# Performance work log

Hardware: AMD Instinct MI355X
Metric: run time of the kernel (lower is better)

Reference implementation:

```python
import jax, jax.numpy as jnp
import numpy as np

EMB = 1024
DM = 64
NH = 16

def setup_inputs() -> dict:
    key = jax.random.key(0)
    ks = jax.random.split(key, 11)
    bs, slen = 2, 2048
    s = 1.0 / np.sqrt(EMB)
    inp = {
        'Q': jax.random.normal(ks[0], (bs, slen, EMB), jnp.float32),
        'K': jax.random.normal(ks[1], (bs, slen, EMB), jnp.float32),
        'V': jax.random.normal(ks[2], (bs, slen, EMB), jnp.float32),
        'Wq': jax.random.normal(ks[3], (EMB, DM * NH), jnp.float32) * s,
        'bq': jnp.zeros((DM * NH,), jnp.float32),
        'Wk': jax.random.normal(ks[4], (EMB, DM * NH), jnp.float32) * s,
        'bk': jnp.zeros((DM * NH,), jnp.float32),
        'Wv': jax.random.normal(ks[5], (EMB, DM * NH), jnp.float32) * s,
        'bv': jnp.zeros((DM * NH,), jnp.float32),
        'Wo': jax.random.normal(ks[6], (DM * NH, EMB), jnp.float32) * (1.0 / np.sqrt(DM * NH)),
        'bo': jnp.zeros((EMB,), jnp.float32),
    }
    return inp

def reference(Q, K, V, Wq, bq, Wk, bk, Wv, bv, Wo, bo):
    bs, q_len, _ = Q.shape
    kv_len = K.shape[1]
    scale = 1.0 / np.sqrt(DM)
    # project and split heads: (n, l, h, d)
    q = (scale * (Q @ Wq + bq)).reshape(bs, q_len, NH, DM)
    k = (K @ Wk + bk).reshape(bs, kv_len, NH, DM)
    v = (V @ Wv + bv).reshape(bs, kv_len, NH, DM)
    # scores (n, h, l, s) -- full S x S matrix, as in the original
    qk = jnp.einsum('nlhd,nshd->nhls', q, k)
    a = jax.nn.softmax(qk, axis=-1)  # dropout p=0 -> identity
    o = jnp.einsum('nhls,nshd->nlhd', a, v).reshape(bs, q_len, NH * DM)
    return o @ Wo + bo
```

## Files before the change

### kernel.cpp

```cpp
#include <hip/hip_runtime.h>
#include <cstdint>
#include <cstddef>

#define EMB  1024
#define DM   64
#define NH   16
#define SLEN 2048
#define BS   2

typedef _Float16 f16x8 __attribute__((ext_vector_type(8)));
typedef _Float16 f16x4 __attribute__((ext_vector_type(4)));
typedef __fp16   hf2   __attribute__((ext_vector_type(2)));
typedef __fp16   hf4   __attribute__((ext_vector_type(4)));
typedef __fp16   hf8   __attribute__((ext_vector_type(8)));
typedef float    f32x4 __attribute__((ext_vector_type(4)));

#define ASYNC_LD16(gp, lp)                                                        \
    __builtin_amdgcn_global_load_lds(                                             \
        (const __attribute__((address_space(1))) void*)(gp),                      \
        (__attribute__((address_space(3))) void*)(lp), 16, 0, 0)

__global__ __launch_bounds__(256)
void prep(const float* __restrict__ Wq, const float* __restrict__ Wk,
          const float* __restrict__ Wv, const float* __restrict__ Wo,
          _Float16* __restrict__ WqT, _Float16* __restrict__ WkT,
          _Float16* __restrict__ WvT, _Float16* __restrict__ WoT)
{
    __shared__ float t[64][65];
    const float* W;
    _Float16*    T;
    switch (blockIdx.z) {
        case 0:  W = Wq; T = WqT; break;
        case 1:  W = Wk; T = WkT; break;
        case 2:  W = Wv; T = WvT; break;
        default: W = Wo; T = WoT; break;
    }
    const int tid = threadIdx.x;
    const int bn  = (blockIdx.x & 15) * 64;
    const int bk  = (blockIdx.x >> 4) * 64;

    #pragma unroll
    for (int p = 0; p < 4; ++p) {
        int row = p * 16 + (tid >> 4);
        int col = (tid & 15) * 4;
        float4 v = *(const float4*)(W + (size_t)(bk + row) * EMB + bn + col);
        t[row][col+0] = v.x; t[row][col+1] = v.y; t[row][col+2] = v.z; t[row][col+3] = v.w;
    }
    __syncthreads();
    #pragma unroll
    for (int p = 0; p < 4; ++p) {
        int nr = p * 16 + (tid >> 4);
        int kc = (tid & 15) * 4;
        f16x4 o;
        o[0] = (_Float16)t[kc+0][nr];
        o[1] = (_Float16)t[kc+1][nr];
        o[2] = (_Float16)t[kc+2][nr];
        o[3] = (_Float16)t[kc+3][nr];
        *(f16x4*)&T[(size_t)(bn + nr) * EMB + bk + kc] = o;
    }
}

template <bool A32>
__device__ __forceinline__
void gemm_core(const void* __restrict__ Aptr, const _Float16* __restrict__ Bt,
               const float* __restrict__ bias, float* __restrict__ Cf,
               _Float16* __restrict__ Ch, int M, int N, int K,
               float scale, int mode, int bx, int by)
{
    __shared__ __align__(16) _Float16 As[2][64 * 64];
    __shared__ __align__(16) _Float16 Bs[2][128 * 64];

    const int tid  = threadIdx.x;
    const int lane = tid & 63;
    const int wave = tid >> 6;
    const int c    = lane & 15;
    const int quad = lane >> 4;
    const int bm   = by * 64;
    const int bn   = bx * 128;
    const int wm   = (wave >> 1) * 32;
    const int wn   = (wave & 1) * 64;

    f32x4 acc[2][4];
    #pragma unroll
    for (int i = 0; i < 2; ++i)
        #pragma unroll
        for (int j = 0; j < 4; ++j)
            #pragma unroll
            for (int r = 0; r < 4; ++r) acc[i][j][r] = 0.f;

    const size_t Kb = (size_t)K * 2;
    const int    lc = ((tid & 7) ^ ((tid >> 3) & 7)) * 16;
    const char* gB = (const char*)Bt + (size_t)(bn + (tid >> 3)) * Kb + lc;

    const char*  gA16 = nullptr;
    const float* gA32 = nullptr;
    int aswz0 = 0, aswz1 = 0;
    if constexpr (A32) {
        const int ar  = tid >> 2;
        const int acg = tid & 3;
        gA32  = (const float*)Aptr + (size_t)(bm + ar) * K + acg * 16;
        aswz0 = ar * 64 + (((2*acg    ) ^ (ar & 7)) * 8);
        aswz1 = ar * 64 + (((2*acg + 1) ^ (ar & 7)) * 8);
    } else {
        gA16 = (const char*)Aptr + (size_t)(bm + (tid >> 3)) * Kb + lc;
    }

    const int NS = K / 64;

    auto stageB = [&](int buf, int t) {
        const size_t ko = (size_t)t * 128;
        char* lB = (char*)&Bs[buf][0] + wave * 1024;
        ASYNC_LD16(gB + ko,           lB);
        ASYNC_LD16(gB + 32*Kb + ko,   lB + 4096);
        ASYNC_LD16(gB + 64*Kb + ko,   lB + 8192);
        ASYNC_LD16(gB + 96*Kb + ko,   lB + 12288);
    };
    auto stageA16 = [&](int buf, int t) {
        const size_t ko = (size_t)t * 128;
        char* lA = (char*)&As[buf][0] + wave * 1024;
        ASYNC_LD16(gA16 + ko,         lA);
        ASYNC_LD16(gA16 + 32*Kb + ko, lA + 4096);
    };
    auto writeA32 = [&](int buf, const float4& a0, const float4& a1,
                        const float4& a2, const float4& a3) {
        f16x8 h0, h1;
        h0[0] = (_Float16)a0.x; h0[1] = (_Float16)a0.y;
        h0[2] = (_Float16)a0.z; h0[3] = (_Float16)a0.w;
        h0[4] = (_Float16)a1.x; h0[5] = (_Float16)a1.y;
        h0[6] = (_Float16)a1.z; h0[7] = (_Float16)a1.w;
        h1[0] = (_Float16)a2.x; h1[1] = (_Float16)a2.y;
        h1[2] = (_Float16)a2.z; h1[3] = (_Float16)a2.w;
        h1[4] = (_Float16)a3.x; h1[5] = (_Float16)a3.y;
        h1[6] = (_Float16)a3.z; h1[7] = (_Float16)a3.w;
        *(f16x8*)&As[buf][aswz0] = h0;
        *(f16x8*)&As[buf][aswz1] = h1;
    };

    if constexpr (A32) {
        float4 a0 = *(const float4*)(gA32 + 0);
        float4 a1 = *(const float4*)(gA32 + 4);
        float4 a2 = *(const float4*)(gA32 + 8);
        float4 a3 = *(const float4*)(gA32 + 12);
        stageB(0, 0);
        writeA32(0, a0, a1, a2, a3);
    } else {
        stageA16(0, 0);
        stageB(0, 0);
    }
    __syncthreads();

    int cur = 0;
    for (int t = 0; t < NS; ++t) {
        float4 a0, a1, a2, a3;
        if constexpr (A32) {
            if (t + 1 < NS) {
                const float* p = gA32 + (size_t)(t + 1) * 64;
                a0 = *(const float4*)(p + 0);
                a1 = *(const float4*)(p + 4);
                a2 = *(const float4*)(p + 8);
                a3 = *(const float4*)(p + 12);
            }
        }
        if (t + 1 < NS) {
            if constexpr (!A32) stageA16(cur ^ 1, t + 1);
            stageB(cur ^ 1, t + 1);
        }

        #pragma unroll
        for (int kk = 0; kk < 2; ++kk) {
            f16x8 af[2], bf[4];
            #pragma unroll
            for (int i = 0; i < 2; ++i)
                af[i] = *(const f16x8*)
                    &As[cur][(wm + i*16 + c) * 64 + (((kk*4 + quad) ^ (c & 7)) * 8)];
            #pragma unroll
            for (int j = 0; j < 4; ++j)
                bf[j] = *(const f16x8*)
                    &Bs[cur][(wn + j*16 + c) * 64 + (((kk*4 + quad) ^ (c & 7)) * 8)];
            #pragma unroll
            for (int i = 0; i < 2; ++i)
                #pragma unroll
                for (int j = 0; j < 4; ++j)
                    acc[i][j] = __builtin_amdgcn_mfma_f32_16x16x32_f16(af[i], bf[j], acc[i][j], 0, 0, 0);
        }

        if constexpr (A32) {
            if (t + 1 < NS) writeA32(cur ^ 1, a0, a1, a2, a3);
        }
        __syncthreads();
        cur ^= 1;
    }

    float bcol[4];
    #pragma unroll
    for (int j = 0; j < 4; ++j) bcol[j] = bias[bn + wn + j * 16 + c];

    #pragma unroll
    for (int i = 0; i < 2; ++i) {
        int m0 = bm + wm + i * 16 + quad * 4;
        #pragma unroll
        for (int j = 0; j < 4; ++j) {
            int n = bn + wn + j * 16 + c;
            if (mode == 0) {
                #pragma unroll
                for (int r = 0; r < 4; ++r)
                    Cf[(size_t)(m0 + r) * N + n] = acc[i][j][r] + bcol[j];
            } else if (mode == 1) {
                int h = n >> 6, d = n & 63;
                #pragma unroll
                for (int r = 0; r < 4; ++r) {
                    int mm = m0 + r;
                    int b = mm >> 11, l = mm & (SLEN - 1);
                    Ch[(((size_t)(b * NH + h)) * SLEN + l) * DM + d] =
                        (_Float16)((acc[i][j][r] + bcol[j]) * scale);
                }
            } else {
                int h = n >> 6, d = n & 63;
                int b = m0 >> 11, l = m0 & (SLEN - 1);
                f16x4 o;
                #pragma unroll
                for (int r = 0; r < 4; ++r)
                    o[r] = (_Float16)(acc[i][j][r] + bcol[j]);
                *(f16x4*)&Ch[(((size_t)(b * NH + h)) * DM + d) * SLEN + l] = o;
            }
        }
    }
}

__device__ __forceinline__ void xcd_swz(int& bx, int& by)
{
    int wid = blockIdx.x + 8 * blockIdx.y;
    bx = wid >> 6;
    by = wid & 63;
}

__global__ __launch_bounds__(256)
void gemm_qkv(const float* __restrict__ Q, const float* __restrict__ K,
              const float* __restrict__ V,
              const _Float16* __restrict__ WqT, const _Float16* __restrict__ WkT,
              const _Float16* __restrict__ WvT,
              const float* __restrict__ bq, const float* __restrict__ bk,
              const float* __restrict__ bv,
              _Float16* __restrict__ q_ws, _Float16* __restrict__ k_ws,
              _Float16* __restrict__ v_ws)
{
    const float* A;
    const _Float16* Bt;
    const float* bias;
    _Float16* Ch;
    float scale;
    int mode;
    if (blockIdx.z == 0)      { A = Q; Bt = WqT; bias = bq; Ch = q_ws; scale = 0.18033688f; mode = 1; }
    else if (blockIdx.z == 1) { A = K; Bt = WkT; bias = bk; Ch = k_ws; scale = 1.0f;        mode = 1; }
    else                      { A = V; Bt = WvT; bias = bv; Ch = v_ws; scale = 1.0f;        mode = 2; }
    int bx, by; xcd_swz(bx, by);
    gemm_core<true>(A, Bt, bias, nullptr, Ch, BS * SLEN, NH * DM, EMB, scale, mode, bx, by);
}

__global__ __launch_bounds__(256)
void gemm_out(const _Float16* __restrict__ Oh, const _Float16* __restrict__ WoT,
              const float* __restrict__ bo, float* __restrict__ out)
{
    int bx, by; xcd_swz(bx, by);
    gemm_core<false>(Oh, WoT, bo, out, nullptr, BS * SLEN, EMB, NH * DM, 1.0f, 0, bx, by);
}

__global__ __launch_bounds__(512)
void attn_mfma(const _Float16* __restrict__ qw, const _Float16* __restrict__ kw,
               const _Float16* __restrict__ vwT, _Float16* __restrict__ ow)
{
    __shared__ __align__(16) _Float16 Kt[4][64 * 64];
    __shared__ __align__(16) _Float16 Vt[4][64 * 64];

    const int tid  = threadIdx.x;
    const int lane = tid & 63;
    const int wave = tid >> 6;
    const int c    = lane & 15;
    const int quad = lane >> 4;
    const int qg   = wave & 3;
    const int kh   = wave >> 2;
    const int bh   = blockIdx.y;
    const int b    = bh >> 4;
    const int h    = bh & 15;
    const int qbase = blockIdx.x * 128 + qg * 32;

    const _Float16* kb = kw  + (size_t)bh * SLEN * DM;
    const _Float16* vb = vwT + (size_t)bh * DM * SLEN;
    const _Float16* qb = qw  + (size_t)bh * SLEN * DM;

    f16x8 qf[2][2];
    #pragma unroll
    for (int t = 0; t < 2; ++t)
        #pragma unroll
        for (int ch = 0; ch < 2; ++ch)
            qf[t][ch] = *(const f16x8*)(qb + (size_t)(qbase + t*16 + c) * DM + ch*32 + quad*8);

    f32x4 oacc[2][4];
    f32x4 lacc[2];
    #pragma unroll
    for (int t = 0; t < 2; ++t) {
        #pragma unroll
        for (int dg = 0; dg < 4; ++dg)
            #pragma unroll
            for (int r = 0; r < 4; ++r) oacc[t][dg][r] = 0.f;
        #pragma unroll
        for (int r = 0; r < 4; ++r) lacc[t][r] = 0.f;
    }

    const f16x8 ones8 = {(_Float16)1.f, (_Float16)1.f, (_Float16)1.f, (_Float16)1.f,
                         (_Float16)1.f, (_Float16)1.f, (_Float16)1.f, (_Float16)1.f};
    const f32x4 zero4 = {0.f, 0.f, 0.f, 0.f};

    const int r0  = wave * 8 + (lane >> 3);
    const int lc0 = (((lane & 7) ^ ((lane >> 3) & 7)) * 16);
    const char* gk = (const char*)kb + r0 * 128 + lc0;
    const char* gv = (const char*)vb + (size_t)r0 * 4096 + lc0;

    auto stage = [&](int buf) {
        char* pk = (char*)&Kt[buf][0] + wave * 1024;
        char* pv = (char*)&Vt[buf][0] + wave * 1024;
        ASYNC_LD16(gk, pk);
        ASYNC_LD16(gv, pv);
        gk += 8192;
        gv += 128;
    };

    stage(0); stage(1); stage(2);
    asm volatile("s_waitcnt vmcnt(4)" ::: "memory");
    __builtin_amdgcn_s_barrier();
    asm volatile("" ::: "memory");

    const int NT = SLEN / 64;
    for (int t = 0; t < NT; ++t) {
        stage((t + 3) & 3);
        const int cb = t & 3;

        f16x8 kf[2][2];
        #pragma unroll
        for (int kg = 0; kg < 2; ++kg)
            #pragma unroll
            for (int ch = 0; ch < 2; ++ch)
                kf[kg][ch] = *(const f16x8*)
                    &Kt[cb][(kh*32 + kg*16 + c) * 64 + (((ch*4 + quad) ^ (c & 7)) * 8)];

        f32x4 s[2][2];
        #pragma unroll
        for (int t2 = 0; t2 < 2; ++t2)
            #pragma unroll
            for (int kg = 0; kg < 2; ++kg) {
                s[t2][kg] = __builtin_amdgcn_mfma_f32_16x16x32_f16(kf[kg][0], qf[t2][0], zero4,     0, 0, 0);
                s[t2][kg] = __builtin_amdgcn_mfma_f32_16x16x32_f16(kf[kg][1], qf[t2][1], s[t2][kg], 0, 0, 0);
            }

        f16x8 pf8[2];
        #pragma unroll
        for (int t2 = 0; t2 < 2; ++t2) {
            hf4 h4[2];
            #pragma unroll
            for (int u = 0; u < 2; ++u) {
                float p0 = __builtin_amdgcn_exp2f(s[t2][u][0]);
                float p1 = __builtin_amdgcn_exp2f(s[t2][u][1]);
                float p2 = __builtin_amdgcn_exp2f(s[t2][u][2]);
                float p3 = __builtin_amdgcn_exp2f(s[t2][u][3]);
                hf2 lo = __builtin_amdgcn_cvt_pkrtz(p0, p1);
                hf2 hi = __builtin_amdgcn_cvt_pkrtz(p2, p3);
                h4[u] = __builtin_shufflevector(lo, hi, 0, 1, 2, 3);
            }
            hf8 h8 = __builtin_shufflevector(h4[0], h4[1], 0, 1, 2, 3, 4, 5, 6, 7);
            pf8[t2] = __builtin_bit_cast(f16x8, h8);
        }

        #pragma unroll
        for (int t2 = 0; t2 < 2; ++t2)
            lacc[t2] = __builtin_amdgcn_mfma_f32_16x16x32_f16(pf8[t2], ones8, lacc[t2], 0, 0, 0);

        #pragma unroll
        for (int dg = 0; dg < 4; ++dg) {
            f16x4 vf[2];
            #pragma unroll
            for (int u = 0; u < 2; ++u)
                vf[u] = *(const f16x4*)
                    &Vt[cb][(dg*16 + c) * 64 +
                            (((kh*4 + 2*u + (quad >> 1)) ^ (c & 7)) * 8) + (quad & 1) * 4];
            f16x8 v8 = __builtin_shufflevector(vf[0], vf[1], 0, 1, 2, 3, 4, 5, 6, 7);
            #pragma unroll
            for (int t2 = 0; t2 < 2; ++t2)
                oacc[t2][dg] = __builtin_amdgcn_mfma_f32_16x16x32_f16(pf8[t2], v8, oacc[t2][dg], 0, 0, 0);
        }

        asm volatile("s_waitcnt vmcnt(4)" ::: "memory");
        __builtin_amdgcn_s_barrier();
        asm volatile("" ::: "memory");
    }

    __syncthreads();

    float* mb = (float*)&Kt[0][0];
    #pragma unroll
    for (int t = 0; t < 2; ++t) {
        if (kh == 1) {
            float* p = mb + ((qg * 64 + lane) * 20);
            *(f32x4*)(p +  0) = oacc[t][0];
            *(f32x4*)(p +  4) = oacc[t][1];
            *(f32x4*)(p +  8) = oacc[t][2];
            *(f32x4*)(p + 12) = oacc[t][3];
            *(f32x4*)(p + 16) = lacc[t];
        }
        __syncthreads();
        if (kh == 0) {
            const float* p = mb + ((qg * 64 + lane) * 20);
            f32x4 po[4], pl;
            po[0] = *(const f32x4*)(p +  0);
            po[1] = *(const f32x4*)(p +  4);
            po[2] = *(const f32x4*)(p +  8);
            po[3] = *(const f32x4*)(p + 12);
            pl    = *(const f32x4*)(p + 16);
            #pragma unroll
            for (int r = 0; r < 4; ++r) {
                float linv = 1.0f / (lacc[t][r] + pl[r]);
                int row = qbase + t*16 + quad*4 + r;
                #pragma unroll
                for (int dg = 0; dg < 4; ++dg)
                    ow[((size_t)b * SLEN + row) * EMB + h * DM + dg*16 + c] =
                        (_Float16)((oacc[t][dg][r] + po[dg][r]) * linv);
            }
        }
        __syncthreads();
    }
}

extern "C" void kernel_launch(void* const* d_in, const int* in_sizes, int n_in,
                              void* d_out, int out_size, void* d_ws, size_t ws_size,
                              hipStream_t stream)
{
    const float* Q  = (const float*)d_in[0];
    const float* K  = (const float*)d_in[1];
    const float* V  = (const float*)d_in[2];
    const float* Wq = (const float*)d_in[3];
    const float* bq = (const float*)d_in[4];
    const float* Wk = (const float*)d_in[5];
    const float* bk = (const float*)d_in[6];
    const float* Wv = (const float*)d_in[7];
    const float* bv = (const float*)d_in[8];
    const float* Wo = (const float*)d_in[9];
    const float* bo = (const float*)d_in[10];
    float* out = (float*)d_out;

    const size_t MN = (size_t)BS * SLEN * NH * DM;
    const size_t WW = (size_t)EMB * NH * DM;

    _Float16* base = (_Float16*)d_ws;
    _Float16* WqT  = base;
    _Float16* WkT  = WqT + WW;
    _Float16* WvT  = WkT + WW;
    _Float16* WoT  = WvT + WW;
    _Float16* q_ws = WoT + WW;
    _Float16* k_ws = q_ws + MN;
    _Float16* v_ws = k_ws + MN;
    _Float16* o_ws = v_ws + MN;

    dim3 blk(256);

    prep<<<dim3(256, 1, 4), blk, 0, stream>>>(Wq, Wk, Wv, Wo,
                                              WqT, WkT, WvT, WoT);

    gemm_qkv<<<dim3(8, 64, 3), blk, 0, stream>>>(Q, K, V, WqT, WkT, WvT,
                                                 bq, bk, bv, q_ws, k_ws, v_ws);

    attn_mfma<<<dim3(SLEN / 128, BS * NH), dim3(512), 0, stream>>>(q_ws, k_ws, v_ws, o_ws);

    gemm_out<<<dim3(8, 64, 1), blk, 0, stream>>>(o_ws, WoT, bo, out);
}
```

Before: 231.5 us.

## Deepen fp32 A prefetch to two stages with manual waitcnt barriers in QKV GEMM

In the QKV projection GEMM, fp32 A tiles are now register-prefetched two k-steps ahead instead of one, and the main loop is fully unrolled over a compile-time K. Plain __syncthreads is replaced by explicit s_waitcnt lgkmcnt/vmcnt plus s_barrier, so the global loads for the tile after next can stay in flight across the barrier. This aims to hide global load latency behind the MFMA work. It costs extra registers for the second prefetch set, and correctness now depends on the hand-written vmcnt counts matching the async load ordering.

```diff
diff --git a/kernel.cpp b/kernel.cpp
--- a/kernel.cpp
+++ b/kernel.cpp
@@ -64,9 +64,12 @@
 __device__ __forceinline__
 void gemm_core(const void* __restrict__ Aptr, const _Float16* __restrict__ Bt,
                const float* __restrict__ bias, float* __restrict__ Cf,
-               _Float16* __restrict__ Ch, int M, int N, int K,
+               _Float16* __restrict__ Ch, int M, int N,
                float scale, int mode, int bx, int by)
 {
+    constexpr int K  = 1024;
+    constexpr int NS = K / 64;
+
     __shared__ __align__(16) _Float16 As[2][64 * 64];
     __shared__ __align__(16) _Float16 Bs[2][128 * 64];
 
@@ -104,8 +107,6 @@
     } else {
         gA16 = (const char*)Aptr + (size_t)(bm + (tid >> 3)) * Kb + lc;
     }
-
-    const int NS = K / 64;
 
     auto stageB = [&](int buf, int t) {
         const size_t ko = (size_t)t * 128;
@@ -121,74 +122,92 @@
         ASYNC_LD16(gA16 + ko,         lA);
         ASYNC_LD16(gA16 + 32*Kb + ko, lA + 4096);
     };
-    auto writeA32 = [&](int buf, const float4& a0, const float4& a1,
-                        const float4& a2, const float4& a3) {
+    auto writeA32 = [&](int buf, const float4* a) {
         f16x8 h0, h1;
-        h0[0] = (_Float16)a0.x; h0[1] = (_Float16)a0.y;
-        h0[2] = (_Float16)a0.z; h0[3] = (_Float16)a0.w;
-        h0[4] = (_Float16)a1.x; h0[5] = (_Float16)a1.y;
-        h0[6] = (_Float16)a1.z; h0[7] = (_Float16)a1.w;
-        h1[0] = (_Float16)a2.x; h1[1] = (_Float16)a2.y;
-        h1[2] = (_Float16)a2.z; h1[3] = (_Float16)a2.w;
-        h1[4] = (_Float16)a3.x; h1[5] = (_Float16)a3.y;
-        h1[6] = (_Float16)a3.z; h1[7] = (_Float16)a3.w;
+        h0[0] = (_Float16)a[0].x; h0[1] = (_Float16)a[0].y;
+        h0[2] = (_Float16)a[0].z; h0[3] = (_Float16)a[0].w;
+        h0[4] = (_Float16)a[1].x; h0[5] = (_Float16)a[1].y;
+        h0[6] = (_Float16)a[1].z; h0[7] = (_Float16)a[1].w;
+        h1[0] = (_Float16)a[2].x; h1[1] = (_Float16)a[2].y;
+        h1[2] = (_Float16)a[2].z; h1[3] = (_Float16)a[2].w;
+        h1[4] = (_Float16)a[3].x; h1[5] = (_Float16)a[3].y;
+        h1[6] = (_Float16)a[3].z; h1[7] = (_Float16)a[3].w;
         *(f16x8*)&As[buf][aswz0] = h0;
         *(f16x8*)&As[buf][aswz1] = h1;
     };
+    auto compute = [&](int cur) {
+        #pragma unroll
+        for (int kk = 0; kk < 2; ++kk) {
+            f16x8 af[2], bf[4];
+            #pragma unroll
+            for (int i = 0; i < 2; ++i)
+                af[i] = *(const f16x8*)
+                    &As[cur][(wm + i*16 + c) * 64 + (((kk*4 + quad) ^ (c & 7)) * 8)];
+            #pragma unroll
+            for (int j = 0; j < 4; ++j)
+                bf[j] = *(const f16x8*)
+                    &Bs[cur][(wn + j*16 + c) * 64 + (((kk*4 + quad) ^ (c & 7)) * 8)];
+            #pragma unroll
+            for (int i = 0; i < 2; ++i)
+                #pragma unroll
+                for (int j = 0; j < 4; ++j)
+                    acc[i][j] = __builtin_amdgcn_mfma_f32_16x16x32_f16(af[i], bf[j], acc[i][j], 0, 0, 0);
+        }
+    };
 
     if constexpr (A32) {
-        float4 a0 = *(const float4*)(gA32 + 0);
-        float4 a1 = *(const float4*)(gA32 + 4);
-        float4 a2 = *(const float4*)(gA32 + 8);
-        float4 a3 = *(const float4*)(gA32 + 12);
-        stageB(0, 0);
-        writeA32(0, a0, a1, a2, a3);
+        float4 pend[4];
+        {
+            float4 c0[4];
+            #pragma unroll
+            for (int i = 0; i < 4; ++i) c0[i] = *(const float4*)(gA32 + i*4);
+            stageB(0, 0);
+            #pragma unroll
+            for (int i = 0; i < 4; ++i) pend[i] = *(const float4*)(gA32 + 64 + i*4);
+            writeA32(0, c0);
+            asm volatile("s_waitcnt lgkmcnt(0)" ::: "memory");
+            asm volatile("s_waitcnt vmcnt(4)" ::: "memory");
+            __builtin_amdgcn_s_barrier();
+            asm volatile("" ::: "memory");
+        }
+        #pragma unroll
+        for (int t = 0; t < NS; ++t) {
+            const int cur = t & 1;
+            if (t + 1 < NS) stageB(cur ^ 1, t + 1);
+            float4 nxt[4];
+            if (t + 2 < NS) {
+                const float* p = gA32 + (size_t)(t + 2) * 64;
+                #pragma unroll
+                for (int i = 0; i < 4; ++i) nxt[i] = *(const float4*)(p + i*4);
+            }
+            compute(cur);
+            if (t + 1 < NS) {
+                writeA32(cur ^ 1, pend);
+                asm volatile("s_waitcnt lgkmcnt(0)" ::: "memory");
+                if (t + 2 < NS) {
+                    asm volatile("s_waitcnt vmcnt(4)" ::: "memory");
+                } else {
+                    asm volatile("s_waitcnt vmcnt(0)" ::: "memory");
+                }
+                __builtin_amdgcn_s_barrier();
+                asm volatile("" ::: "memory");
+                if (t + 2 < NS) {
+                    #pragma unroll
+                    for (int i = 0; i < 4; ++i) pend[i] = nxt[i];
+                }
+            }
+        }
     } else {
         stageA16(0, 0);
         stageB(0, 0);
-    }
-    __syncthreads();
-
-    int cur = 0;
-    for (int t = 0; t < NS; ++t) {
-        float4 a0, a1, a2, a3;
-        if constexpr (A32) {
-            if (t + 1 < NS) {
-                const float* p = gA32 + (size_t)(t + 1) * 64;
-                a0 = *(const float4*)(p + 0);
-                a1 = *(const float4*)(p + 4);
-                a2 = *(const float4*)(p + 8);
-                a3 = *(const float4*)(p + 12);
-            }
-        }
-        if (t + 1 < NS) {
-            if constexpr (!A32) stageA16(cur ^ 1, t + 1);
-            stageB(cur ^ 1, t + 1);
-        }
-
-        #pragma unroll
-        for (int kk = 0; kk < 2; ++kk) {
-            f16x8 af[2], bf[4];
-            #pragma unroll
-            for (int i = 0; i < 2; ++i)
-                af[i] = *(const f16x8*)
-                    &As[cur][(wm + i*16 + c) * 64 + (((kk*4 + quad) ^ (c & 7)) * 8)];
-            #pragma unroll
-            for (int j = 0; j < 4; ++j)
-                bf[j] = *(const f16x8*)
-                    &Bs[cur][(wn + j*16 + c) * 64 + (((kk*4 + quad) ^ (c & 7)) * 8)];
-            #pragma unroll
-            for (int i = 0; i < 2; ++i)
-                #pragma unroll
-                for (int j = 0; j < 4; ++j)
-                    acc[i][j] = __builtin_amdgcn_mfma_f32_16x16x32_f16(af[i], bf[j], acc[i][j], 0, 0, 0);
-        }
-
-        if constexpr (A32) {
-            if (t + 1 < NS) writeA32(cur ^ 1, a0, a1, a2, a3);
-        }
         __syncthreads();
-        cur ^= 1;
+        int cur = 0;
+        for (int t = 0; t < NS; ++t) {
+            if (t + 1 < NS) { stageA16(cur ^ 1, t + 1); stageB(cur ^ 1, t + 1); }
+            compute(cur);
+            __syncthreads();
+            cur ^= 1;
+        }
     }
 
     float bcol[4];
@@ -254,7 +273,7 @@
     else if (blockIdx.z == 1) { A = K; Bt = WkT; bias = bk; Ch = k_ws; scale = 1.0f;        mode = 1; }
     else                      { A = V; Bt = WvT; bias = bv; Ch = v_ws; scale = 1.0f;        mode = 2; }
     int bx, by; xcd_swz(bx, by);
-    gemm_core<true>(A, Bt, bias, nullptr, Ch, BS * SLEN, NH * DM, EMB, scale, mode, bx, by);
+    gemm_core<true>(A, Bt, bias, nullptr, Ch, BS * SLEN, NH * DM, scale, mode, bx, by);
 }
 
 __global__ __launch_bounds__(256)
@@ -262,7 +281,7 @@
               const float* __restrict__ bo, float* __restrict__ out)
 {
     int bx, by; xcd_swz(bx, by);
-    gemm_core<false>(Oh, WoT, bo, out, nullptr, BS * SLEN, EMB, NH * DM, 1.0f, 0, bx, by);
+    gemm_core<false>(Oh, WoT, bo, out, nullptr, BS * SLEN, EMB, 1.0f, 0, bx, by);
 }
 
 __global__ __launch_bounds__(512)
```

Result: faster. 225.6 us (-2.5%).
